# Kernel optimization log

Hardware: AMD Instinct MI355X
Metric: run time of the kernel (lower is better)

Reference implementation:

```python
import jax, jax.numpy as jnp
import numpy as np

# direction id -> (lat_shift, lon_shift)
WIND_DIRS = [(0, 0), (-1, 0), (-1, 1), (0, 1), (1, 1), (1, 0), (1, -1), (0, -1), (-1, -1)]
SWIN_SHIFT = (1, 3, 6)       # (pl, lat, lon)
WIND_SHIFT_SCALE = 2
LAT_REGIONS, LON_REGIONS = 4, 8
NUM_DIRS = 9


def setup_inputs() -> dict:
    key = jax.random.key(0)
    k1, k2 = jax.random.split(key)
    x = jax.random.normal(k1, (2, 14, 128, 256, 96), dtype=jnp.float32)
    wind_direction_id = jax.random.randint(k2, (2, 128, 256), 0, NUM_DIRS)
    return {"x": x, "wind_direction_id": wind_direction_id}


def _regional_dominant_dirs(wid):
    # wid: (B, H, W) int -> (B, LAT_REGIONS, LON_REGIONS) dominant direction per region
    B, H, W = wid.shape
    r = wid.reshape(B, LAT_REGIONS, H // LAT_REGIONS, LON_REGIONS, W // LON_REGIONS)
    counts = jnp.sum(jax.nn.one_hot(r, NUM_DIRS, dtype=jnp.float32), axis=(2, 4))  # (B, latR, lonR, 9)
    return jnp.argmax(counts, axis=-1)  # ties -> first max, matching torch bincount().argmax()


def reference(x, wind_direction_id):
    # x: (B, Pl, Lat, Lon, C); wind_direction_id: (B, H, W) in [0, 9)
    B, Pl, Lat, Lon, C = x.shape
    # 1) Swin fixed shift (negative roll on Pl, Lat, Lon)
    sp, sl, so = SWIN_SHIFT
    x = jnp.roll(x, (-sp, -sl, -so), axis=(1, 2, 3))
    # 2) per-region dominant wind direction
    rd = _regional_dominant_dirs(wind_direction_id)  # (B, latR, lonR)
    # nearest-neighbor upsample to full grid (matches F.interpolate mode='nearest')
    ih = (jnp.arange(Lat) * LAT_REGIONS) // Lat
    iw = (jnp.arange(Lon) * LON_REGIONS) // Lon
    dirs_up = rd[:, ih][:, :, iw]  # (B, Lat, Lon)
    # 3) mask & combine over the 9 rolled versions
    combined = jnp.zeros_like(x)
    for dir_id, (lat_s, lon_s) in enumerate(WIND_DIRS):
        als, alo = lat_s * WIND_SHIFT_SCALE, lon_s * WIND_SHIFT_SCALE
        shifted = x if (als == 0 and alo == 0) else jnp.roll(x, (als, alo), axis=(2, 3))
        mask = (dirs_up == dir_id).astype(x.dtype)[:, None, :, :, None]  # (B,1,Lat,Lon,1)
        combined = combined + shifted * mask
    # 4) global dominant direction (returned as stat)
    counts = jnp.bincount(wind_direction_id.reshape(-1), length=NUM_DIRS)
    dominant_id = jnp.argmax(counts)
    return combined, dominant_id
```

## Files before the change

### kernel.cpp

```cpp
#include <hip/hip_runtime.h>

namespace {
constexpr int kB   = 2;
constexpr int kPl  = 14;
constexpr int kLat = 128;
constexpr int kLon = 256;
constexpr int kC   = 96;
constexpr int kNumDirs = 9;
constexpr int kC4  = kC / 4;
constexpr int kNTotal = kB * kPl * kLat * kLon * kC;
constexpr int kN4 = kNTotal / 4;
constexpr int kRegions = kB * 4 * 8;
constexpr int kCopyBlocks = 1024;
constexpr int kItersPerThread = kN4 / (kCopyBlocks * 256);
}

typedef float f4 __attribute__((ext_vector_type(4)));

__device__ __constant__ int c_lat_s[kNumDirs] = {0,-1,-1, 0, 1, 1, 1, 0,-1};
__device__ __constant__ int c_lon_s[kNumDirs] = {0, 0, 1, 1, 1, 0,-1,-1,-1};

__global__ __launch_bounds__(256) void region_dirs_kernel(
        const int* __restrict__ wid, int* __restrict__ rdpack,
        int* __restrict__ cnt_blk) {
    __shared__ int cnt[kNumDirs];
    const int t = threadIdx.x;
    if (t < kNumDirs) cnt[t] = 0;
    __syncthreads();

    const int blk  = blockIdx.x;
    const int rlon = blk & 7;
    const int rlat = (blk >> 3) & 3;
    const int b    = blk >> 5;

    for (int k = t; k < 1024; k += 256) {
        const int i  = k >> 5;
        const int j  = k & 31;
        const int la = rlat * 32 + i;
        const int lo = rlon * 32 + j;
        atomicAdd(&cnt[wid[(b * kLat + la) * kLon + lo]], 1);
    }
    __syncthreads();

    if (t < kNumDirs) cnt_blk[blk * kNumDirs + t] = cnt[t];
    if (t == 0) {
        int best = 0, bestc = cnt[0];
        #pragma unroll
        for (int d = 1; d < kNumDirs; ++d)
            if (cnt[d] > bestc) { bestc = cnt[d]; best = d; }
        const int dla = 3 - 2 * c_lat_s[best];
        const int dlo = 6 - 2 * c_lon_s[best];
        rdpack[blk] = (dla << 8) | dlo;
    }
}

__global__ __launch_bounds__(256) void gather_kernel(
        const f4* __restrict__ x, const int* __restrict__ rdpack,
        const int* __restrict__ cnt_blk, f4* __restrict__ out,
        float* __restrict__ out_dom) {
    if (blockIdx.x == kCopyBlocks) {
        __shared__ int tot[kNumDirs];
        const int t = threadIdx.x;
        if (t < kNumDirs) {
            int s = 0;
            for (int r = 0; r < kRegions; ++r) s += cnt_blk[r * kNumDirs + t];
            tot[t] = s;
        }
        __syncthreads();
        if (t == 0) {
            int best = 0, bestc = tot[0];
            #pragma unroll
            for (int d = 1; d < kNumDirs; ++d)
                if (tot[d] > bestc) { bestc = tot[d]; best = d; }
            *out_dom = (float)best;
        }
        return;
    }

    const int base = blockIdx.x * 256 + threadIdx.x;
    constexpr int kStride = kCopyBlocks * 256;

    #pragma unroll 4
    for (int k = 0; k < kItersPerThread; ++k) {
        const int i = base + k * kStride;
        const int c4 = i % kC4;
        int r = i / kC4;
        const int lo = r & (kLon - 1); r >>= 8;
        const int la = r & (kLat - 1); r >>= 7;
        const int p  = r % kPl;
        const int b  = r / kPl;

        const int pack = rdpack[(b * 4 + (la >> 5)) * 8 + (lo >> 5)];
        const int lasrc = (la + (pack >> 8)) & (kLat - 1);
        const int losrc = (lo + (pack & 0xff)) & (kLon - 1);
        int psrc = p + 1; if (psrc >= kPl) psrc = 0;

        const int src = (((b * kPl + psrc) * kLat + lasrc) * kLon + losrc) * kC4 + c4;
        const f4 v = __builtin_nontemporal_load(&x[src]);
        __builtin_nontemporal_store(v, &out[i]);
    }
}

extern "C" void kernel_launch(void* const* d_in, const int* in_sizes, int n_in,
                              void* d_out, int out_size, void* d_ws, size_t ws_size,
                              hipStream_t stream) {
    const float* x   = (const float*)d_in[0];
    const int*   wid = (const int*)d_in[1];
    float* out = (float*)d_out;

    int* rdpack  = (int*)d_ws;
    int* cnt_blk = rdpack + kRegions;

    region_dirs_kernel<<<kRegions, 256, 0, stream>>>(wid, rdpack, cnt_blk);
    gather_kernel<<<kCopyBlocks + 1, 256, 0, stream>>>(
        (const f4*)x, rdpack, cnt_blk, (f4*)out, out + kNTotal);
}
```

Measured before the change: 140.9 us.

## Assign one output row per block and cache region directions in shared memory

The grid-stride gather is replaced by one block per (b, pl, lat) output row, so 3584 blocks each copy a contiguous 256x96 float row. Each block computes the batch, level and latitude indices once and preloads the 8 regional shift codes into shared memory. This removes per-element div/mod index decoding and the repeated global rdpack loads. In exchange there are many more small blocks and a __syncthreads per block; the memory traffic stays the same.

```diff
diff --git a/kernel.cpp b/kernel.cpp
--- a/kernel.cpp
+++ b/kernel.cpp
@@ -9,10 +9,10 @@
 constexpr int kNumDirs = 9;
 constexpr int kC4  = kC / 4;
 constexpr int kNTotal = kB * kPl * kLat * kLon * kC;
-constexpr int kN4 = kNTotal / 4;
 constexpr int kRegions = kB * 4 * 8;
-constexpr int kCopyBlocks = 1024;
-constexpr int kItersPerThread = kN4 / (kCopyBlocks * 256);
+constexpr int kRowTasks = kB * kPl * kLat;
+constexpr int kRowF4 = kLon * kC4;
+constexpr int kRowIters = kRowF4 / 256;
 }
 
 typedef float f4 __attribute__((ext_vector_type(4)));
@@ -54,11 +54,11 @@
     }
 }
 
-__global__ __launch_bounds__(256) void gather_kernel(
+__global__ __launch_bounds__(256) void gather_rows_kernel(
         const f4* __restrict__ x, const int* __restrict__ rdpack,
         const int* __restrict__ cnt_blk, f4* __restrict__ out,
         float* __restrict__ out_dom) {
-    if (blockIdx.x == kCopyBlocks) {
+    if (blockIdx.x == kRowTasks) {
         __shared__ int tot[kNumDirs];
         const int t = threadIdx.x;
         if (t < kNumDirs) {
@@ -77,27 +77,34 @@
         return;
     }
 
-    const int base = blockIdx.x * 256 + threadIdx.x;
-    constexpr int kStride = kCopyBlocks * 256;
+    const int t   = threadIdx.x;
+    const int blk = blockIdx.x;
+    const int la  = blk & (kLat - 1);
+    const int bp  = blk >> 7;
+    const int p   = bp % kPl;
+    const int b   = bp / kPl;
+    int psrc = p + 1; if (psrc >= kPl) psrc = 0;
 
-    #pragma unroll 4
-    for (int k = 0; k < kItersPerThread; ++k) {
-        const int i = base + k * kStride;
-        const int c4 = i % kC4;
-        int r = i / kC4;
-        const int lo = r & (kLon - 1); r >>= 8;
-        const int la = r & (kLat - 1); r >>= 7;
-        const int p  = r % kPl;
-        const int b  = r / kPl;
+    __shared__ int s_pack8[8];
+    if (t < 8) s_pack8[t] = rdpack[(b * 4 + (la >> 5)) * 8 + t];
+    __syncthreads();
 
-        const int pack = rdpack[(b * 4 + (la >> 5)) * 8 + (lo >> 5)];
+    const long srow = (long)((b * kPl + psrc) * kLat) * kRowF4;
+    const long drow = (long)blk * kRowF4;
+
+    #pragma unroll 6
+    for (int k = 0; k < kRowIters; ++k) {
+        const int flat = k * 256 + t;
+        const int lo   = flat / kC4;
+        const int c4   = flat - lo * kC4;
+
+        const int pack  = s_pack8[lo >> 5];
         const int lasrc = (la + (pack >> 8)) & (kLat - 1);
         const int losrc = (lo + (pack & 0xff)) & (kLon - 1);
-        int psrc = p + 1; if (psrc >= kPl) psrc = 0;
 
-        const int src = (((b * kPl + psrc) * kLat + lasrc) * kLon + losrc) * kC4 + c4;
+        const long src = srow + (long)lasrc * kRowF4 + losrc * kC4 + c4;
         const f4 v = __builtin_nontemporal_load(&x[src]);
-        __builtin_nontemporal_store(v, &out[i]);
+        __builtin_nontemporal_store(v, &out[drow + flat]);
     }
 }
 
@@ -112,6 +119,6 @@
     int* cnt_blk = rdpack + kRegions;
 
     region_dirs_kernel<<<kRegions, 256, 0, stream>>>(wid, rdpack, cnt_blk);
-    gather_kernel<<<kCopyBlocks + 1, 256, 0, stream>>>(
+    gather_rows_kernel<<<kRowTasks + 1, 256, 0, stream>>>(
         (const f4*)x, rdpack, cnt_blk, (f4*)out, out + kNTotal);
 }
```

After: 133.9 us. -5.0%, faster.
